# Optimization experiments

Hardware: AMD Instinct MI355X
Metric: run time of the kernel (lower is better)

Reference implementation:

```python
import jax, jax.numpy as jnp
import numpy as np

N_LOC = 100000
N_EVT = 100000
N_EDGE = 1600000
F_LOC = 128
F_EVT = 128
QID_DIM = 16
QID_BUCKETS = 4096
HID = 64


def setup_inputs() -> dict:
    key = jax.random.key(0)
    ks = jax.random.split(key, 16)
    s = 0.05
    emb = jax.random.normal(ks[4], (QID_BUCKETS + 1, QID_DIM), jnp.float32) * s
    emb = emb.at[0].set(0.0)  # padding_idx=0
    return {
        "loc_feat": jax.random.normal(ks[0], (N_LOC, F_LOC), jnp.float32),
        "evt_feat": jax.random.normal(ks[1], (N_EVT, F_EVT), jnp.float32),
        "qid_bucket": jax.random.randint(ks[2], (N_LOC,), 0, QID_BUCKETS + 1),
        "edge_index": jax.random.randint(ks[3], (2, N_EDGE), 0, N_LOC),
        "emb": emb,
        "W_loc": jax.random.normal(ks[5], (F_LOC + QID_DIM, HID), jnp.float32) * s,
        "b_loc": jnp.zeros((HID,), jnp.float32),
        "W_evt": jax.random.normal(ks[6], (F_EVT, HID), jnp.float32) * s,
        "b_evt": jnp.zeros((HID,), jnp.float32),
        "W_l": jax.random.normal(ks[7], (HID, HID), jnp.float32) * s,
        "b_l": jnp.zeros((HID,), jnp.float32),
        "W_r": jax.random.normal(ks[8], (HID, HID), jnp.float32) * s,
        "W_h1": jax.random.normal(ks[9], (HID, HID // 2), jnp.float32) * s,
        "b_h1": jnp.zeros((HID // 2,), jnp.float32),
        "W_h2": jax.random.normal(ks[10], (HID // 2, 1), jnp.float32) * s,
        "b_h2": jnp.zeros((1,), jnp.float32),
    }


def reference(loc_feat, evt_feat, qid_bucket, edge_index, emb,
              W_loc, b_loc, W_evt, b_evt, W_l, b_l, W_r,
              W_h1, b_h1, W_h2, b_h2):
    # location input = [x || qid_embedding]
    loc_in = jnp.concatenate([loc_feat, emb[qid_bucket]], axis=1)
    loc_x = jax.nn.relu(loc_in @ W_loc + b_loc)          # [N_loc, H]
    evt_x = jax.nn.relu(evt_feat @ W_evt + b_evt)        # [N_evt, H]

    src, dst = edge_index[0], edge_index[1]
    msg = evt_x[src]                                     # [E, H] gather
    summed = jax.ops.segment_sum(msg, dst, num_segments=N_LOC)
    cnt = jax.ops.segment_sum(jnp.ones((msg.shape[0],), msg.dtype), dst,
                              num_segments=N_LOC)
    mean = summed / jnp.maximum(cnt, 1.0)[:, None]       # scatter-mean aggr

    # SAGEConv: lin_l(mean of neighbors) + lin_r(self)
    loc_x = jax.nn.relu(mean @ W_l + b_l + loc_x @ W_r)

    h = jax.nn.relu(loc_x @ W_h1 + b_h1)
    logits = (h @ W_h2 + b_h2)[:, 0]
    return logits
```

## Files before the change

kernel.cpp:

```cpp
#include <hip/hip_runtime.h>

#define N_LOC 100000
#define N_EVT 100000
#define N_EDGE 1600000
#define NB 391
#define NBIN 391
#define SEGCAP 48
#define BCAPP 9216
#define TILE 4096
#define RBLK 64
#define DGRID 1563

typedef short bf16x8 __attribute__((ext_vector_type(8)));
typedef float f32x4  __attribute__((ext_vector_type(4)));

__device__ __forceinline__ unsigned bf16_rne(float x) {
    unsigned u = __float_as_uint(x);
    return (u + 0x7fffu + ((u >> 16) & 1u)) >> 16;
}
__device__ __forceinline__ float bf_lo(unsigned u) { return __uint_as_float(u << 16); }
__device__ __forceinline__ float bf_hi(unsigned u) { return __uint_as_float(u & 0xffff0000u); }

__global__ __launch_bounds__(256) void k_front(
    const float* __restrict__ evt_feat, const float* __restrict__ W_evt,
    const float* __restrict__ b_evt, unsigned short* __restrict__ evtb,
    const float* __restrict__ loc_feat, const int* __restrict__ qid,
    const float* __restrict__ emb, const float* __restrict__ W_loc,
    const float* __restrict__ b_loc, unsigned short* __restrict__ locxb,
    const int* __restrict__ ei, int* __restrict__ cntm,
    unsigned* __restrict__ seg, unsigned* __restrict__ dummy_row)
{
    __shared__ __align__(16) unsigned char smem[43008];
    const int bid = blockIdx.x;
    const int t = threadIdx.x;

    if (bid < NBIN) {
        int* h = (int*)smem;
        if (bid == 0 && t < 32) dummy_row[t] = 0u;
        for (int i = t; i < NB; i += 256) h[i] = 0;
        __syncthreads();
        const int e0 = bid * TILE;
        int srcv[16], dstv[16], rnk[16];
#pragma unroll
        for (int j = 0; j < 16; ++j) {
            int e = e0 + j * 256 + t;
            if (e < N_EDGE) {
                srcv[j] = ei[e];
                dstv[j] = ei[N_EDGE + e];
                rnk[j] = atomicAdd(&h[dstv[j] >> 8], 1);
            }
        }
        __syncthreads();
        for (int i = t; i < NB; i += 256)
            cntm[(size_t)bid * NB + i] = min(h[i], SEGCAP);
#pragma unroll
        for (int j = 0; j < 16; ++j) {
            int e = e0 + j * 256 + t;
            if (e < N_EDGE && rnk[j] < SEGCAP)
                seg[((size_t)bid * NB + (dstv[j] >> 8)) * SEGCAP + rnk[j]] =
                    (unsigned)srcv[j] | ((unsigned)(dstv[j] & 255) << 24);
        }
        return;
    }

    const int lane = t & 63;
    const int w = t >> 6;
    const int colL = lane & 15;
    const int kq = lane >> 4;

    int db = bid - NBIN;
    if (db < DGRID) {
        unsigned short* sA = (unsigned short*)smem;
        unsigned short* sB = sA + 64 * 136;
        const int gbase = db * RBLK;
        for (int idx = t; idx < 4096; idx += 256) {
            int kp = idx >> 6, c = idx & 63;
            float w0 = W_evt[(2 * kp + 0) * 64 + c];
            float w1 = W_evt[(2 * kp + 1) * 64 + c];
            *(unsigned*)&sB[c * 136 + 2 * kp] = bf16_rne(w0) | (bf16_rne(w1) << 16);
        }
        for (int idx = t; idx < RBLK * 32; idx += 256) {
            int row = idx >> 5, c4 = idx & 31;
            int grow = gbase + row;
            float4 v = (grow < N_EVT) ? ((const float4*)evt_feat)[(size_t)grow * 32 + c4]
                                      : make_float4(0.f, 0.f, 0.f, 0.f);
            uint2 p = make_uint2(bf16_rne(v.x) | (bf16_rne(v.y) << 16),
                                 bf16_rne(v.z) | (bf16_rne(v.w) << 16));
            *(uint2*)&sA[row * 136 + c4 * 4] = p;
        }
        __syncthreads();
        f32x4 acc0 = {0.f, 0.f, 0.f, 0.f}, acc1 = acc0, acc2 = acc0, acc3 = acc0;
#pragma unroll
        for (int s = 0; s < 4; ++s) {
            const int kb = s * 32 + kq * 8;
            bf16x8 a  = *(const bf16x8*)&sA[(16 * w + colL) * 136 + kb];
            bf16x8 b0 = *(const bf16x8*)&sB[(colL +  0) * 136 + kb];
            bf16x8 b1 = *(const bf16x8*)&sB[(colL + 16) * 136 + kb];
            bf16x8 b2 = *(const bf16x8*)&sB[(colL + 32) * 136 + kb];
            bf16x8 b3 = *(const bf16x8*)&sB[(colL + 48) * 136 + kb];
            acc0 = __builtin_amdgcn_mfma_f32_16x16x32_bf16(a, b0, acc0, 0, 0, 0);
            acc1 = __builtin_amdgcn_mfma_f32_16x16x32_bf16(a, b1, acc1, 0, 0, 0);
            acc2 = __builtin_amdgcn_mfma_f32_16x16x32_bf16(a, b2, acc2, 0, 0, 0);
            acc3 = __builtin_amdgcn_mfma_f32_16x16x32_bf16(a, b3, acc3, 0, 0, 0);
        }
        const float bias0 = b_evt[colL +  0];
        const float bias1 = b_evt[colL + 16];
        const float bias2 = b_evt[colL + 32];
        const float bias3 = b_evt[colL + 48];
        const int rbase = gbase + 16 * w + kq * 4;
#pragma unroll
        for (int j = 0; j < 4; ++j) {
            int grow = rbase + j;
            if (grow < N_EVT) {
                size_t o = (size_t)grow * 64;
                evtb[o + colL +  0] = (unsigned short)bf16_rne(fmaxf(acc0[j] + bias0, 0.f));
                evtb[o + colL + 16] = (unsigned short)bf16_rne(fmaxf(acc1[j] + bias1, 0.f));
                evtb[o + colL + 32] = (unsigned short)bf16_rne(fmaxf(acc2[j] + bias2, 0.f));
                evtb[o + colL + 48] = (unsigned short)bf16_rne(fmaxf(acc3[j] + bias3, 0.f));
            }
        }
        return;
    }

    {
        db -= DGRID;
        unsigned short* sA = (unsigned short*)smem;
        unsigned short* sB = sA + 64 * 168;
        const int gbase = db * RBLK;
        for (int idx = t; idx < 72 * 64; idx += 256) {
            int kp = idx >> 6, c = idx & 63;
            float w0 = W_loc[(2 * kp + 0) * 64 + c];
            float w1 = W_loc[(2 * kp + 1) * 64 + c];
            *(unsigned*)&sB[c * 168 + 2 * kp] = bf16_rne(w0) | (bf16_rne(w1) << 16);
        }
        for (int idx = t; idx < 64 * 2; idx += 256) {
            int c = idx >> 1, h2 = idx & 1;
            *(uint4*)&sB[c * 168 + 144 + h2 * 8] = make_uint4(0, 0, 0, 0);
        }
        for (int idx = t; idx < RBLK * 32; idx += 256) {
            int row = idx >> 5, c4 = idx & 31;
            int grow = gbase + row;
            float4 v = (grow < N_LOC) ? ((const float4*)loc_feat)[(size_t)grow * 32 + c4]
                                      : make_float4(0.f, 0.f, 0.f, 0.f);
            uint2 p = make_uint2(bf16_rne(v.x) | (bf16_rne(v.y) << 16),
                                 bf16_rne(v.z) | (bf16_rne(v.w) << 16));
            *(uint2*)&sA[row * 168 + c4 * 4] = p;
        }
        for (int idx = t; idx < RBLK * 4; idx += 256) {
            int row = idx >> 2, e4 = idx & 3;
            int grow = gbase + row;
            int q = (grow < N_LOC) ? qid[grow] : 0;
            float4 v = ((const float4*)emb)[(size_t)q * 4 + e4];
            uint2 p = make_uint2(bf16_rne(v.x) | (bf16_rne(v.y) << 16),
                                 bf16_rne(v.z) | (bf16_rne(v.w) << 16));
            *(uint2*)&sA[row * 168 + 128 + e4 * 4] = p;
        }
        for (int idx = t; idx < RBLK * 2; idx += 256) {
            int row = idx >> 1, h2 = idx & 1;
            *(uint4*)&sA[row * 168 + 144 + h2 * 8] = make_uint4(0, 0, 0, 0);
        }
        __syncthreads();
        f32x4 acc0 = {0.f, 0.f, 0.f, 0.f}, acc1 = acc0, acc2 = acc0, acc3 = acc0;
#pragma unroll
        for (int s = 0; s < 5; ++s) {
            const int kb = s * 32 + kq * 8;
            bf16x8 a  = *(const bf16x8*)&sA[(16 * w + colL) * 168 + kb];
            bf16x8 b0 = *(const bf16x8*)&sB[(colL +  0) * 168 + kb];
            bf16x8 b1 = *(const bf16x8*)&sB[(colL + 16) * 168 + kb];
            bf16x8 b2 = *(const bf16x8*)&sB[(colL + 32) * 168 + kb];
            bf16x8 b3 = *(const bf16x8*)&sB[(colL + 48) * 168 + kb];
            acc0 = __builtin_amdgcn_mfma_f32_16x16x32_bf16(a, b0, acc0, 0, 0, 0);
            acc1 = __builtin_amdgcn_mfma_f32_16x16x32_bf16(a, b1, acc1, 0, 0, 0);
            acc2 = __builtin_amdgcn_mfma_f32_16x16x32_bf16(a, b2, acc2, 0, 0, 0);
            acc3 = __builtin_amdgcn_mfma_f32_16x16x32_bf16(a, b3, acc3, 0, 0, 0);
        }
        const float bias0 = b_loc[colL +  0];
        const float bias1 = b_loc[colL + 16];
        const float bias2 = b_loc[colL + 32];
        const float bias3 = b_loc[colL + 48];
        const int rbase = gbase + 16 * w + kq * 4;
#pragma unroll
        for (int j = 0; j < 4; ++j) {
            int grow = rbase + j;
            if (grow < N_LOC) {
                size_t o = (size_t)grow * 64;
                locxb[o + colL +  0] = (unsigned short)bf16_rne(fmaxf(acc0[j] + bias0, 0.f));
                locxb[o + colL + 16] = (unsigned short)bf16_rne(fmaxf(acc1[j] + bias1, 0.f));
                locxb[o + colL + 32] = (unsigned short)bf16_rne(fmaxf(acc2[j] + bias2, 0.f));
                locxb[o + colL + 48] = (unsigned short)bf16_rne(fmaxf(acc3[j] + bias3, 0.f));
            }
        }
    }
}

__global__ __launch_bounds__(256) void k_bfill(const int* __restrict__ cntm,
                                               const unsigned* __restrict__ seg,
                                               int* __restrict__ deg,
                                               int* __restrict__ row_ex,
                                               int* __restrict__ csr) {
    __shared__ int cnt0[NBIN];
    __shared__ int degl[256];
    __shared__ int sc[256];
    __shared__ int cur[256];
    const int b = blockIdx.x;
    const int t = threadIdx.x;
    for (int i = t; i < NBIN; i += 256) cnt0[i] = cntm[(size_t)i * NB + b];
    degl[t] = 0;
    __syncthreads();
    for (int blk = t; blk < NBIN; blk += 256) {
        const int c = cnt0[blk];
        const unsigned* s = seg + ((size_t)blk * NB + b) * SEGCAP;
        for (int j = 0; j < c; ++j) atomicAdd(&degl[s[j] >> 24], 1);
    }
    __syncthreads();
    const int v = degl[t];
    const int vpad = (v + 15) & ~15;
    sc[t] = vpad;
    __syncthreads();
    for (int off = 1; off < 256; off <<= 1) {
        int x = (t >= off) ? sc[t - off] : 0;
        __syncthreads();
        sc[t] += x;
        __syncthreads();
    }
    const int ex = b * BCAPP + sc[t] - vpad;
    const int loc = b * 256 + t;
    if (loc < N_LOC) { deg[loc] = v; row_ex[loc] = ex; }
    cur[t] = ex;
    __syncthreads();
    for (int blk = t; blk < NBIN; blk += 256) {
        const int c = cnt0[blk];
        const unsigned* s = seg + ((size_t)blk * NB + b) * SEGCAP;
        for (int j = 0; j < c; ++j) {
            unsigned u = s[j];
            int pos = atomicAdd(&cur[u >> 24], 1);
            csr[pos] = (int)(u & 0x00FFFFFFu);
        }
    }
    for (int j = v; j < vpad; ++j) csr[ex + j] = N_EVT;
}

__global__ __launch_bounds__(256, 8) void k_aggr(const unsigned* __restrict__ evtb,
                                                 const int* __restrict__ row_ex,
                                                 const int* __restrict__ deg,
                                                 const int* __restrict__ csr,
                                                 unsigned* __restrict__ meanb, int n) {
    const int lane = threadIdx.x & 63;
    int wid = (blockIdx.x * 256 + threadIdx.x) >> 6;
    wid = __builtin_amdgcn_readfirstlane(wid);
    if (wid >= n) return;
    const int beg = row_ex[wid];
    const int cnt = deg[wid];
    const int cntp = (cnt + 15) & ~15;
    const int half = lane >> 5;
    const int c = lane & 31;
    float a0 = 0.0f, a1 = 0.0f;
    for (int i = 0; i < cntp; i += 16) {
        const int bb = beg + i + half;
        int s0 = csr[bb +  0];
        int s1 = csr[bb +  2];
        int s2 = csr[bb +  4];
        int s3 = csr[bb +  6];
        int s4 = csr[bb +  8];
        int s5 = csr[bb + 10];
        int s6 = csr[bb + 12];
        int s7 = csr[bb + 14];
        unsigned u0 = evtb[(size_t)s0 * 32 + c];
        unsigned u1 = evtb[(size_t)s1 * 32 + c];
        unsigned u2 = evtb[(size_t)s2 * 32 + c];
        unsigned u3 = evtb[(size_t)s3 * 32 + c];
        unsigned u4 = evtb[(size_t)s4 * 32 + c];
        unsigned u5 = evtb[(size_t)s5 * 32 + c];
        unsigned u6 = evtb[(size_t)s6 * 32 + c];
        unsigned u7 = evtb[(size_t)s7 * 32 + c];
        a0 += ((bf_lo(u0) + bf_lo(u1)) + (bf_lo(u2) + bf_lo(u3))) +
              ((bf_lo(u4) + bf_lo(u5)) + (bf_lo(u6) + bf_lo(u7)));
        a1 += ((bf_hi(u0) + bf_hi(u1)) + (bf_hi(u2) + bf_hi(u3))) +
              ((bf_hi(u4) + bf_hi(u5)) + (bf_hi(u6) + bf_hi(u7)));
    }
    a0 += __shfl_xor(a0, 32);
    a1 += __shfl_xor(a1, 32);
    const float inv = 1.0f / (float)max(cnt, 1);
    if (lane < 32)
        meanb[(size_t)wid * 32 + c] = bf16_rne(a0 * inv) | (bf16_rne(a1 * inv) << 16);
}

__global__ __launch_bounds__(256) void k_comb(
    const unsigned* __restrict__ meanb, const unsigned* __restrict__ locxb,
    const float* __restrict__ W_l, const float* __restrict__ b_l,
    const float* __restrict__ W_r,
    const float* __restrict__ W_h1, const float* __restrict__ b_h1,
    const float* __restrict__ W_h2, const float* __restrict__ b_h2,
    float* __restrict__ out, int n)
{
    __shared__ unsigned short sA[64 * 136];
    __shared__ unsigned short sBc[64 * 136];
    __shared__ unsigned short sX[64 * 72];
    __shared__ unsigned short sBh[32 * 72];
    const int t = threadIdx.x;
    const int gbase = blockIdx.x * RBLK;
    for (int idx = t; idx < 64 * 64; idx += 256) {
        int kp = idx >> 6, c = idx & 63;
        float w0, w1;
        if (kp < 32) { w0 = W_l[(2 * kp + 0) * 64 + c]; w1 = W_l[(2 * kp + 1) * 64 + c]; }
        else { w0 = W_r[(2 * kp - 64 + 0) * 64 + c]; w1 = W_r[(2 * kp - 64 + 1) * 64 + c]; }
        *(unsigned*)&sBc[c * 136 + 2 * kp] = bf16_rne(w0) | (bf16_rne(w1) << 16);
    }
    for (int idx = t; idx < 32 * 32; idx += 256) {
        int kp = idx >> 5, c = idx & 31;
        float w0 = W_h1[(2 * kp + 0) * 32 + c];
        float w1 = W_h1[(2 * kp + 1) * 32 + c];
        *(unsigned*)&sBh[c * 72 + 2 * kp] = bf16_rne(w0) | (bf16_rne(w1) << 16);
    }
    for (int idx = t; idx < RBLK * 32; idx += 256) {
        int row = idx >> 5, q = idx & 31;
        int grow = gbase + row;
        uint2 p = make_uint2(0, 0);
        if (grow < n) {
            p = (q < 16) ? ((const uint2*)meanb)[(size_t)grow * 16 + q]
                         : ((const uint2*)locxb)[(size_t)grow * 16 + (q - 16)];
        }
        *(uint2*)&sA[row * 136 + q * 4] = p;
    }
    __syncthreads();
    const int lane = t & 63;
    const int w = t >> 6;
    const int colL = lane & 15;
    const int kq = lane >> 4;
    f32x4 acc0 = {0.f, 0.f, 0.f, 0.f}, acc1 = acc0, acc2 = acc0, acc3 = acc0;
#pragma unroll
    for (int s = 0; s < 4; ++s) {
        const int kb = s * 32 + kq * 8;
        bf16x8 a  = *(const bf16x8*)&sA[(16 * w + colL) * 136 + kb];
        bf16x8 b0 = *(const bf16x8*)&sBc[(colL +  0) * 136 + kb];
        bf16x8 b1 = *(const bf16x8*)&sBc[(colL + 16) * 136 + kb];
        bf16x8 b2 = *(const bf16x8*)&sBc[(colL + 32) * 136 + kb];
        bf16x8 b3 = *(const bf16x8*)&sBc[(colL + 48) * 136 + kb];
        acc0 = __builtin_amdgcn_mfma_f32_16x16x32_bf16(a, b0, acc0, 0, 0, 0);
        acc1 = __builtin_amdgcn_mfma_f32_16x16x32_bf16(a, b1, acc1, 0, 0, 0);
        acc2 = __builtin_amdgcn_mfma_f32_16x16x32_bf16(a, b2, acc2, 0, 0, 0);
        acc3 = __builtin_amdgcn_mfma_f32_16x16x32_bf16(a, b3, acc3, 0, 0, 0);
    }
    {
        const float bias0 = b_l[colL +  0];
        const float bias1 = b_l[colL + 16];
        const float bias2 = b_l[colL + 32];
        const float bias3 = b_l[colL + 48];
#pragma unroll
        for (int j = 0; j < 4; ++j) {
            int row = 16 * w + kq * 4 + j;
            sX[row * 72 + colL +  0] = (unsigned short)bf16_rne(fmaxf(acc0[j] + bias0, 0.f));
            sX[row * 72 + colL + 16] = (unsigned short)bf16_rne(fmaxf(acc1[j] + bias1, 0.f));
            sX[row * 72 + colL + 32] = (unsigned short)bf16_rne(fmaxf(acc2[j] + bias2, 0.f));
            sX[row * 72 + colL + 48] = (unsigned short)bf16_rne(fmaxf(acc3[j] + bias3, 0.f));
        }
    }
    f32x4 h0 = {0.f, 0.f, 0.f, 0.f}, h1 = h0;
#pragma unroll
    for (int s = 0; s < 2; ++s) {
        const int kb = s * 32 + kq * 8;
        bf16x8 a  = *(const bf16x8*)&sX[(16 * w + colL) * 72 + kb];
        bf16x8 b0 = *(const bf16x8*)&sBh[(colL +  0) * 72 + kb];
        bf16x8 b1 = *(const bf16x8*)&sBh[(colL + 16) * 72 + kb];
        h0 = __builtin_amdgcn_mfma_f32_16x16x32_bf16(a, b0, h0, 0, 0, 0);
        h1 = __builtin_amdgcn_mfma_f32_16x16x32_bf16(a, b1, h1, 0, 0, 0);
    }
    {
        const float bh1c0 = b_h1[colL];
        const float bh1c1 = b_h1[colL + 16];
        const float wh2c0 = W_h2[colL];
        const float wh2c1 = W_h2[colL + 16];
        const float bh2 = b_h2[0];
#pragma unroll
        for (int j = 0; j < 4; ++j) {
            float p = fmaxf(h0[j] + bh1c0, 0.f) * wh2c0 +
                      fmaxf(h1[j] + bh1c1, 0.f) * wh2c1;
            p += __shfl_xor(p, 1);
            p += __shfl_xor(p, 2);
            p += __shfl_xor(p, 4);
            p += __shfl_xor(p, 8);
            int grow = gbase + 16 * w + kq * 4 + j;
            if (colL == 0 && grow < n) out[grow] = p + bh2;
        }
    }
}

extern "C" void kernel_launch(void* const* d_in, const int* in_sizes, int n_in,
                              void* d_out, int out_size, void* d_ws, size_t ws_size,
                              hipStream_t stream) {
    const float* loc_feat = (const float*)d_in[0];
    const float* evt_feat = (const float*)d_in[1];
    const int*   qid      = (const int*)d_in[2];
    const int*   ei       = (const int*)d_in[3];
    const float* emb      = (const float*)d_in[4];
    const float* W_loc    = (const float*)d_in[5];
    const float* b_loc    = (const float*)d_in[6];
    const float* W_evt    = (const float*)d_in[7];
    const float* b_evt    = (const float*)d_in[8];
    const float* W_l      = (const float*)d_in[9];
    const float* b_l      = (const float*)d_in[10];
    const float* W_r      = (const float*)d_in[11];
    const float* W_h1     = (const float*)d_in[12];
    const float* b_h1     = (const float*)d_in[13];
    const float* W_h2     = (const float*)d_in[14];
    const float* b_h2     = (const float*)d_in[15];
    float* out = (float*)d_out;

    char* ws = (char*)d_ws;
    size_t off = 0;
    auto alloc = [&](size_t bytes) -> void* {
        void* p = ws + off;
        off += (bytes + 255) & ~(size_t)255;
        return p;
    };
    unsigned* evtb  = (unsigned*)alloc((size_t)(N_EVT + 1) * 32 * 4);
    unsigned* locxb = (unsigned*)alloc((size_t)N_LOC * 32 * 4);
    unsigned* meanb = (unsigned*)alloc((size_t)N_LOC * 32 * 4);
    unsigned* seg   = (unsigned*)alloc((size_t)NBIN * NB * SEGCAP * 4);
    int*   cntm     = (int*)alloc((size_t)NBIN * NB * 4);
    int*   deg      = (int*)alloc((size_t)N_LOC * 4);
    int*   row_ex   = (int*)alloc((size_t)(N_LOC + 1) * 4);
    int*   csr      = (int*)alloc((size_t)NB * BCAPP * 4);
    (void)ws_size; (void)in_sizes; (void)n_in; (void)out_size;

    k_front<<<NBIN + 2 * DGRID, 256, 0, stream>>>(
        evt_feat, W_evt, b_evt, (unsigned short*)evtb,
        loc_feat, qid, emb, W_loc, b_loc, (unsigned short*)locxb,
        ei, cntm, seg, evtb + (size_t)N_EVT * 32);
    k_bfill<<<NB, 256, 0, stream>>>(cntm, seg, deg, row_ex, csr);
    k_aggr<<<N_LOC / 4, 256, 0, stream>>>(evtb, row_ex, deg, csr, meanb, N_LOC);
    k_comb<<<DGRID, 256, 0, stream>>>(meanb, locxb, W_l, b_l, W_r,
                                      W_h1, b_h1, W_h2, b_h2, out, N_LOC);
}
```

Measured before the change: 124.3 us.

## Pre-transpose weights once and replace capped segment bins with compact prefix-sum binning

```diff
diff --git a/kernel.cpp b/kernel.cpp
--- a/kernel.cpp
+++ b/kernel.cpp
@@ -5,7 +5,6 @@
 #define N_EDGE 1600000
 #define NB 391
 #define NBIN 391
-#define SEGCAP 48
 #define BCAPP 9216
 #define TILE 4096
 #define RBLK 64
@@ -21,22 +20,63 @@
 __device__ __forceinline__ float bf_lo(unsigned u) { return __uint_as_float(u << 16); }
 __device__ __forceinline__ float bf_hi(unsigned u) { return __uint_as_float(u & 0xffff0000u); }
 
+__global__ __launch_bounds__(256) void k_prep(
+    const float* __restrict__ W_evt, const float* __restrict__ W_loc,
+    const float* __restrict__ W_l, const float* __restrict__ W_r,
+    const float* __restrict__ W_h1,
+    unsigned short* __restrict__ Wt_evt,
+    unsigned short* __restrict__ Wt_loc,
+    unsigned short* __restrict__ Wt_c,
+    unsigned short* __restrict__ Wt_h1,
+    unsigned* __restrict__ dummy_row)
+{
+    const int t = threadIdx.x;
+    for (int idx = t; idx < 64 * 64; idx += 256) {
+        int kp = idx >> 6, c = idx & 63;
+        *(unsigned*)&Wt_evt[c * 128 + 2 * kp] =
+            bf16_rne(W_evt[(2 * kp + 0) * 64 + c]) |
+            (bf16_rne(W_evt[(2 * kp + 1) * 64 + c]) << 16);
+    }
+    for (int idx = t; idx < 80 * 64; idx += 256) {
+        int kp = idx >> 6, c = idx & 63;
+        unsigned v = 0;
+        if (kp < 72)
+            v = bf16_rne(W_loc[(2 * kp + 0) * 64 + c]) |
+                (bf16_rne(W_loc[(2 * kp + 1) * 64 + c]) << 16);
+        *(unsigned*)&Wt_loc[c * 160 + 2 * kp] = v;
+    }
+    for (int idx = t; idx < 64 * 64; idx += 256) {
+        int kp = idx >> 6, c = idx & 63;
+        float w0, w1;
+        if (kp < 32) { w0 = W_l[(2 * kp + 0) * 64 + c]; w1 = W_l[(2 * kp + 1) * 64 + c]; }
+        else { w0 = W_r[(2 * kp - 64 + 0) * 64 + c]; w1 = W_r[(2 * kp - 64 + 1) * 64 + c]; }
+        *(unsigned*)&Wt_c[c * 128 + 2 * kp] = bf16_rne(w0) | (bf16_rne(w1) << 16);
+    }
+    for (int idx = t; idx < 32 * 32; idx += 256) {
+        int kp = idx >> 5, c = idx & 31;
+        *(unsigned*)&Wt_h1[c * 64 + 2 * kp] =
+            bf16_rne(W_h1[(2 * kp + 0) * 32 + c]) |
+            (bf16_rne(W_h1[(2 * kp + 1) * 32 + c]) << 16);
+    }
+    if (t < 32) dummy_row[t] = 0u;
+}
+
 __global__ __launch_bounds__(256) void k_front(
-    const float* __restrict__ evt_feat, const float* __restrict__ W_evt,
+    const float* __restrict__ evt_feat, const unsigned short* __restrict__ Wt_evt,
     const float* __restrict__ b_evt, unsigned short* __restrict__ evtb,
     const float* __restrict__ loc_feat, const int* __restrict__ qid,
-    const float* __restrict__ emb, const float* __restrict__ W_loc,
+    const float* __restrict__ emb, const unsigned short* __restrict__ Wt_loc,
     const float* __restrict__ b_loc, unsigned short* __restrict__ locxb,
-    const int* __restrict__ ei, int* __restrict__ cntm,
-    unsigned* __restrict__ seg, unsigned* __restrict__ dummy_row)
+    const int* __restrict__ ei, int* __restrict__ cntm, int* __restrict__ offm,
+    unsigned* __restrict__ binned)
 {
-    __shared__ __align__(16) unsigned char smem[43008];
+    __shared__ __align__(16) unsigned char smem[21504];
     const int bid = blockIdx.x;
     const int t = threadIdx.x;
 
     if (bid < NBIN) {
-        int* h = (int*)smem;
-        if (bid == 0 && t < 32) dummy_row[t] = 0u;
+        int* h  = (int*)smem;
+        int* sh = (int*)(smem + 1600);
         for (int i = t; i < NB; i += 256) h[i] = 0;
         __syncthreads();
         const int e0 = bid * TILE;
@@ -51,14 +91,29 @@
             }
         }
         __syncthreads();
-        for (int i = t; i < NB; i += 256)
-            cntm[(size_t)bid * NB + i] = min(h[i], SEGCAP);
+        sh[t] = (t < NB) ? h[t] : 0;
+        sh[t + 256] = (t + 256 < NB) ? h[t + 256] : 0;
+        __syncthreads();
+        for (int off = 1; off < 512; off <<= 1) {
+            int v0 = (t >= off) ? sh[t - off] : 0;
+            int v1 = (t + 256 >= off) ? sh[t + 256 - off] : 0;
+            __syncthreads();
+            sh[t] += v0;
+            sh[t + 256] += v1;
+            __syncthreads();
+        }
+        for (int i = t; i < NB; i += 256) {
+            cntm[(size_t)bid * NB + i] = h[i];
+            offm[(size_t)bid * NB + i] = sh[i] - h[i];
+        }
 #pragma unroll
         for (int j = 0; j < 16; ++j) {
             int e = e0 + j * 256 + t;
-            if (e < N_EDGE && rnk[j] < SEGCAP)
-                seg[((size_t)bid * NB + (dstv[j] >> 8)) * SEGCAP + rnk[j]] =
+            if (e < N_EDGE) {
+                int bk = dstv[j] >> 8;
+                binned[(size_t)bid * TILE + (sh[bk] - h[bk]) + rnk[j]] =
                     (unsigned)srcv[j] | ((unsigned)(dstv[j] & 255) << 24);
+            }
         }
         return;
     }
@@ -71,14 +126,7 @@
     int db = bid - NBIN;
     if (db < DGRID) {
         unsigned short* sA = (unsigned short*)smem;
-        unsigned short* sB = sA + 64 * 136;
         const int gbase = db * RBLK;
-        for (int idx = t; idx < 4096; idx += 256) {
-            int kp = idx >> 6, c = idx & 63;
-            float w0 = W_evt[(2 * kp + 0) * 64 + c];
-            float w1 = W_evt[(2 * kp + 1) * 64 + c];
-            *(unsigned*)&sB[c * 136 + 2 * kp] = bf16_rne(w0) | (bf16_rne(w1) << 16);
-        }
         for (int idx = t; idx < RBLK * 32; idx += 256) {
             int row = idx >> 5, c4 = idx & 31;
             int grow = gbase + row;
@@ -94,10 +142,10 @@
         for (int s = 0; s < 4; ++s) {
             const int kb = s * 32 + kq * 8;
             bf16x8 a  = *(const bf16x8*)&sA[(16 * w + colL) * 136 + kb];
-            bf16x8 b0 = *(const bf16x8*)&sB[(colL +  0) * 136 + kb];
-            bf16x8 b1 = *(const bf16x8*)&sB[(colL + 16) * 136 + kb];
-            bf16x8 b2 = *(const bf16x8*)&sB[(colL + 32) * 136 + kb];
-            bf16x8 b3 = *(const bf16x8*)&sB[(colL + 48) * 136 + kb];
+            bf16x8 b0 = *(const bf16x8*)&Wt_evt[(colL +  0) * 128 + kb];
+            bf16x8 b1 = *(const bf16x8*)&Wt_evt[(colL + 16) * 128 + kb];
+            bf16x8 b2 = *(const bf16x8*)&Wt_evt[(colL + 32) * 128 + kb];
+            bf16x8 b3 = *(const bf16x8*)&Wt_evt[(colL + 48) * 128 + kb];
             acc0 = __builtin_amdgcn_mfma_f32_16x16x32_bf16(a, b0, acc0, 0, 0, 0);
             acc1 = __builtin_amdgcn_mfma_f32_16x16x32_bf16(a, b1, acc1, 0, 0, 0);
             acc2 = __builtin_amdgcn_mfma_f32_16x16x32_bf16(a, b2, acc2, 0, 0, 0);
@@ -125,18 +173,7 @@
     {
         db -= DGRID;
         unsigned short* sA = (unsigned short*)smem;
-        unsigned short* sB = sA + 64 * 168;
         const int gbase = db * RBLK;
-        for (int idx = t; idx < 72 * 64; idx += 256) {
-            int kp = idx >> 6, c = idx & 63;
-            float w0 = W_loc[(2 * kp + 0) * 64 + c];
-            float w1 = W_loc[(2 * kp + 1) * 64 + c];
-            *(unsigned*)&sB[c * 168 + 2 * kp] = bf16_rne(w0) | (bf16_rne(w1) << 16);
-        }
-        for (int idx = t; idx < 64 * 2; idx += 256) {
-            int c = idx >> 1, h2 = idx & 1;
-            *(uint4*)&sB[c * 168 + 144 + h2 * 8] = make_uint4(0, 0, 0, 0);
-        }
         for (int idx = t; idx < RBLK * 32; idx += 256) {
             int row = idx >> 5, c4 = idx & 31;
             int grow = gbase + row;
@@ -165,10 +202,10 @@
         for (int s = 0; s < 5; ++s) {
             const int kb = s * 32 + kq * 8;
             bf16x8 a  = *(const bf16x8*)&sA[(16 * w + colL) * 168 + kb];
-            bf16x8 b0 = *(const bf16x8*)&sB[(colL +  0) * 168 + kb];
-            bf16x8 b1 = *(const bf16x8*)&sB[(colL + 16) * 168 + kb];
-            bf16x8 b2 = *(const bf16x8*)&sB[(colL + 32) * 168 + kb];
-            bf16x8 b3 = *(const bf16x8*)&sB[(colL + 48) * 168 + kb];
+            bf16x8 b0 = *(const bf16x8*)&Wt_loc[(colL +  0) * 160 + kb];
+            bf16x8 b1 = *(const bf16x8*)&Wt_loc[(colL + 16) * 160 + kb];
+            bf16x8 b2 = *(const bf16x8*)&Wt_loc[(colL + 32) * 160 + kb];
+            bf16x8 b3 = *(const bf16x8*)&Wt_loc[(colL + 48) * 160 + kb];
             acc0 = __builtin_amdgcn_mfma_f32_16x16x32_bf16(a, b0, acc0, 0, 0, 0);
             acc1 = __builtin_amdgcn_mfma_f32_16x16x32_bf16(a, b1, acc1, 0, 0, 0);
             acc2 = __builtin_amdgcn_mfma_f32_16x16x32_bf16(a, b2, acc2, 0, 0, 0);
@@ -194,22 +231,27 @@
 }
 
 __global__ __launch_bounds__(256) void k_bfill(const int* __restrict__ cntm,
-                                               const unsigned* __restrict__ seg,
+                                               const int* __restrict__ offm,
+                                               const unsigned* __restrict__ binned,
                                                int* __restrict__ deg,
                                                int* __restrict__ row_ex,
                                                int* __restrict__ csr) {
     __shared__ int cnt0[NBIN];
+    __shared__ int off0[NBIN];
     __shared__ int degl[256];
     __shared__ int sc[256];
     __shared__ int cur[256];
     const int b = blockIdx.x;
     const int t = threadIdx.x;
-    for (int i = t; i < NBIN; i += 256) cnt0[i] = cntm[(size_t)i * NB + b];
+    for (int i = t; i < NBIN; i += 256) {
+        cnt0[i] = cntm[(size_t)i * NB + b];
+        off0[i] = offm[(size_t)i * NB + b];
+    }
     degl[t] = 0;
     __syncthreads();
     for (int blk = t; blk < NBIN; blk += 256) {
         const int c = cnt0[blk];
-        const unsigned* s = seg + ((size_t)blk * NB + b) * SEGCAP;
+        const unsigned* s = binned + (size_t)blk * TILE + off0[blk];
         for (int j = 0; j < c; ++j) atomicAdd(&degl[s[j] >> 24], 1);
     }
     __syncthreads();
@@ -230,7 +272,7 @@
     __syncthreads();
     for (int blk = t; blk < NBIN; blk += 256) {
         const int c = cnt0[blk];
-        const unsigned* s = seg + ((size_t)blk * NB + b) * SEGCAP;
+        const unsigned* s = binned + (size_t)blk * TILE + off0[blk];
         for (int j = 0; j < c; ++j) {
             unsigned u = s[j];
             int pos = atomicAdd(&cur[u >> 24], 1);
@@ -287,31 +329,15 @@
 
 __global__ __launch_bounds__(256) void k_comb(
     const unsigned* __restrict__ meanb, const unsigned* __restrict__ locxb,
-    const float* __restrict__ W_l, const float* __restrict__ b_l,
-    const float* __restrict__ W_r,
-    const float* __restrict__ W_h1, const float* __restrict__ b_h1,
+    const unsigned short* __restrict__ Wt_c, const float* __restrict__ b_l,
+    const unsigned short* __restrict__ Wt_h1, const float* __restrict__ b_h1,
     const float* __restrict__ W_h2, const float* __restrict__ b_h2,
     float* __restrict__ out, int n)
 {
     __shared__ unsigned short sA[64 * 136];
-    __shared__ unsigned short sBc[64 * 136];
     __shared__ unsigned short sX[64 * 72];
-    __shared__ unsigned short sBh[32 * 72];
     const int t = threadIdx.x;
     const int gbase = blockIdx.x * RBLK;
-    for (int idx = t; idx < 64 * 64; idx += 256) {
-        int kp = idx >> 6, c = idx & 63;
-        float w0, w1;
-        if (kp < 32) { w0 = W_l[(2 * kp + 0) * 64 + c]; w1 = W_l[(2 * kp + 1) * 64 + c]; }
-        else { w0 = W_r[(2 * kp - 64 + 0) * 64 + c]; w1 = W_r[(2 * kp - 64 + 1) * 64 + c]; }
-        *(unsigned*)&sBc[c * 136 + 2 * kp] = bf16_rne(w0) | (bf16_rne(w1) << 16);
-    }
-    for (int idx = t; idx < 32 * 32; idx += 256) {
-        int kp = idx >> 5, c = idx & 31;
-        float w0 = W_h1[(2 * kp + 0) * 32 + c];
-        float w1 = W_h1[(2 * kp + 1) * 32 + c];
-        *(unsigned*)&sBh[c * 72 + 2 * kp] = bf16_rne(w0) | (bf16_rne(w1) << 16);
-    }
     for (int idx = t; idx < RBLK * 32; idx += 256) {
         int row = idx >> 5, q = idx & 31;
         int grow = gbase + row;
@@ -332,10 +358,10 @@
     for (int s = 0; s < 4; ++s) {
         const int kb = s * 32 + kq * 8;
         bf16x8 a  = *(const bf16x8*)&sA[(16 * w + colL) * 136 + kb];
-        bf16x8 b0 = *(const bf16x8*)&sBc[(colL +  0) * 136 + kb];
-        bf16x8 b1 = *(const bf16x8*)&sBc[(colL + 16) * 136 + kb];
-        bf16x8 b2 = *(const bf16x8*)&sBc[(colL + 32) * 136 + kb];
-        bf16x8 b3 = *(const bf16x8*)&sBc[(colL + 48) * 136 + kb];
+        bf16x8 b0 = *(const bf16x8*)&Wt_c[(colL +  0) * 128 + kb];
+        bf16x8 b1 = *(const bf16x8*)&Wt_c[(colL + 16) * 128 + kb];
+        bf16x8 b2 = *(const bf16x8*)&Wt_c[(colL + 32) * 128 + kb];
+        bf16x8 b3 = *(const bf16x8*)&Wt_c[(colL + 48) * 128 + kb];
         acc0 = __builtin_amdgcn_mfma_f32_16x16x32_bf16(a, b0, acc0, 0, 0, 0);
         acc1 = __builtin_amdgcn_mfma_f32_16x16x32_bf16(a, b1, acc1, 0, 0, 0);
         acc2 = __builtin_amdgcn_mfma_f32_16x16x32_bf16(a, b2, acc2, 0, 0, 0);
@@ -360,8 +386,8 @@
     for (int s = 0; s < 2; ++s) {
         const int kb = s * 32 + kq * 8;
         bf16x8 a  = *(const bf16x8*)&sX[(16 * w + colL) * 72 + kb];
-        bf16x8 b0 = *(const bf16x8*)&sBh[(colL +  0) * 72 + kb];
-        bf16x8 b1 = *(const bf16x8*)&sBh[(colL + 16) * 72 + kb];
+        bf16x8 b0 = *(const bf16x8*)&Wt_h1[(colL +  0) * 64 + kb];
+        bf16x8 b1 = *(const bf16x8*)&Wt_h1[(colL + 16) * 64 + kb];
         h0 = __builtin_amdgcn_mfma_f32_16x16x32_bf16(a, b0, h0, 0, 0, 0);
         h1 = __builtin_amdgcn_mfma_f32_16x16x32_bf16(a, b1, h1, 0, 0, 0);
     }
@@ -416,19 +442,27 @@
     unsigned* evtb  = (unsigned*)alloc((size_t)(N_EVT + 1) * 32 * 4);
     unsigned* locxb = (unsigned*)alloc((size_t)N_LOC * 32 * 4);
     unsigned* meanb = (unsigned*)alloc((size_t)N_LOC * 32 * 4);
-    unsigned* seg   = (unsigned*)alloc((size_t)NBIN * NB * SEGCAP * 4);
+    unsigned* binned= (unsigned*)alloc((size_t)NBIN * TILE * 4);
     int*   cntm     = (int*)alloc((size_t)NBIN * NB * 4);
+    int*   offm     = (int*)alloc((size_t)NBIN * NB * 4);
     int*   deg      = (int*)alloc((size_t)N_LOC * 4);
     int*   row_ex   = (int*)alloc((size_t)(N_LOC + 1) * 4);
     int*   csr      = (int*)alloc((size_t)NB * BCAPP * 4);
+    unsigned short* Wt_evt = (unsigned short*)alloc(64 * 128 * 2);
+    unsigned short* Wt_loc = (unsigned short*)alloc(64 * 160 * 2);
+    unsigned short* Wt_c   = (unsigned short*)alloc(64 * 128 * 2);
+    unsigned short* Wt_h1  = (unsigned short*)alloc(32 * 64 * 2);
     (void)ws_size; (void)in_sizes; (void)n_in; (void)out_size;
 
+    k_prep<<<1, 256, 0, stream>>>(W_evt, W_loc, W_l, W_r, W_h1,
+                                  Wt_evt, Wt_loc, Wt_c, Wt_h1,
+                                  evtb + (size_t)N_EVT * 32);
     k_front<<<NBIN + 2 * DGRID, 256, 0, stream>>>(
-        evt_feat, W_evt, b_evt, (unsigned short*)evtb,
-        loc_feat, qid, emb, W_loc, b_loc, (unsigned short*)locxb,
-        ei, cntm, seg, evtb + (size_t)N_EVT * 32);
-    k_bfill<<<NB, 256, 0, stream>>>(cntm, seg, deg, row_ex, csr);
+        evt_feat, Wt_evt, b_evt, (unsigned short*)evtb,
+        loc_feat, qid, emb, Wt_loc, b_loc, (unsigned short*)locxb,
+        ei, cntm, offm, binned);
+    k_bfill<<<NB, 256, 0, stream>>>(cntm, offm, binned, deg, row_ex, csr);
     k_aggr<<<N_LOC / 4, 256, 0, stream>>>(evtb, row_ex, deg, csr, meanb, N_LOC);
-    k_comb<<<DGRID, 256, 0, stream>>>(meanb, locxb, W_l, b_l, W_r,
-                                      W_h1, b_h1, W_h2, b_h2, out, N_LOC);
-}
+    k_comb<<<DGRID, 256, 0, stream>>>(meanb, locxb, Wt_c, b_l, Wt_h1, b_h1,
+                                      W_h2, b_h2, out, N_LOC);
+}
```

Result: slower. 148.8 us (+19.7%).
